# Kernel optimization log

Hardware: AMD Instinct MI355X
Metric: run time of the kernel (lower is better)

The kernel has to match this reference:

```python
import jax, jax.numpy as jnp
import numpy as np

B, IN, NC, O, H = 256, 2048, 1000, 4096, 4  # batch, in_features, num_classes, n_decoders, hidden
NEG_SLOPE = 0.1

def setup_inputs() -> dict:
    key = jax.random.key(0)
    ks = jax.random.split(key, 7)
    s1 = 1.0 / np.sqrt(IN)
    s2 = 1.0 / np.sqrt(H)
    return {
        "x":   jax.random.normal(ks[0], (B, IN), jnp.float32),
        "fcW": jax.random.normal(ks[1], (NC, IN), jnp.float32) * s1,
        "fcb": jax.random.normal(ks[2], (NC,), jnp.float32) * s1,
        "W1":  jax.random.normal(ks[3], (O, IN, H), jnp.float32) * s1,
        "b1":  jax.random.normal(ks[4], (O, H), jnp.float32) * s1,
        "W2":  jax.random.normal(ks[5], (O, H), jnp.float32) * s2,
        "b2":  jax.random.normal(ks[6], (O,), jnp.float32) * s2,
    }

def reference(x, fcW, fcb, W1, b1, W2, b2):
    # fc head: x1 = x @ fcW^T + fcb  -> [B, NC]
    x1 = jnp.einsum("bi,ci->bc", x, fcW) + fcb
    # 4096 tiny MLPs batched into one grouped GEMM:
    # h = leaky_relu(x @ W1_o + b1_o) for each decoder o  -> [B, O, H]
    h = jnp.einsum("bi,oih->boh", x, W1) + b1
    h = jnp.where(h >= 0, h, NEG_SLOPE * h)
    # second layer (H->1) collapses to a weighted reduction -> [B, O]
    x2 = jnp.einsum("boh,oh->bo", h, W2) + b2
    return (x1, x2)
```

## Files before the change

kernel.cpp:

```cpp
#include <hip/hip_runtime.h>


typedef __bf16 bf16_t;
typedef __bf16 bf16x8 __attribute__((ext_vector_type(8)));
typedef __bf16 bf16x4 __attribute__((ext_vector_type(4)));
typedef float  f32x4  __attribute__((ext_vector_type(4)));

#define LDSTR 72

__global__ __launch_bounds__(256, 4)
void fused_dual(const float* __restrict__ x,
                const float* __restrict__ fcW,
                const float* __restrict__ fcb,
                const float* __restrict__ W1,
                const float* __restrict__ b1,
                const float* __restrict__ W2,
                const float* __restrict__ b2,
                float* __restrict__ out)
{
    __shared__ bf16_t lA[64 * LDSTR];
    __shared__ bf16_t lB[64 * LDSTR];

    const int tid = threadIdx.x;
    const int blk = blockIdx.x;
    const int cg  = blk >> 2;
    const int rg  = blk & 3;
    const int m0  = rg * 64;
    const bool is_fc = (cg < 16);
    const int c0  = (is_fc ? cg : cg - 16) * 64;

    const int a_row = tid >> 4;
    const int a_c4  = tid & 15;
    const int b_n  = tid >> 2;
    const int b_kb = tid & 3;

    const float* ap = x + (m0 + a_row) * 2048 + a_c4 * 4;
    const float* bp;
    if (is_fc) {
        int row = c0 + b_n; if (row > 999) row = 999;
        bp = fcW + row * 2048 + b_kb * 16;
    } else {
        const int o = (c0 >> 2) + (b_n >> 2);
        bp = W1 + o * 8192 + b_kb * 64 + (b_n & 3);
    }

    float4 aR[4];
    float  bR[16];

    #pragma unroll
    for (int r = 0; r < 4; ++r) aR[r] = *(const float4*)(ap + r * (16 * 2048));
    if (is_fc) {
        #pragma unroll
        for (int q = 0; q < 4; ++q) {
            float4 t = *(const float4*)(bp + q * 4);
            bR[q*4+0] = t.x; bR[q*4+1] = t.y; bR[q*4+2] = t.z; bR[q*4+3] = t.w;
        }
    } else {
        #pragma unroll
        for (int j = 0; j < 16; ++j) bR[j] = bp[j * 4];
    }

    const int wav  = tid >> 6;
    const int lane = tid & 63;
    const int l15  = lane & 15;
    const int quad = lane >> 4;

    f32x4 acc[4];
    #pragma unroll
    for (int nt = 0; nt < 4; ++nt) acc[nt] = (f32x4){0.f, 0.f, 0.f, 0.f};

    char* lAb = (char*)lA;
    char* lBb = (char*)lB;
    const int aW = (a_row) * (LDSTR * 2) + a_c4 * 8;
    const int bW = b_n * (LDSTR * 2) + b_kb * 32;

    for (int kt = 0; kt < 32; ++kt) {
        __syncthreads();
        #pragma unroll
        for (int r = 0; r < 4; ++r) {
            bf16x4 v;
            v[0] = (bf16_t)aR[r].x; v[1] = (bf16_t)aR[r].y;
            v[2] = (bf16_t)aR[r].z; v[3] = (bf16_t)aR[r].w;
            *(bf16x4*)(lAb + aW + r * (16 * LDSTR * 2)) = v;
        }
        {
            bf16x8 v0, v1;
            #pragma unroll
            for (int j = 0; j < 8; ++j) { v0[j] = (bf16_t)bR[j]; v1[j] = (bf16_t)bR[8 + j]; }
            *(bf16x8*)(lBb + bW)      = v0;
            *(bf16x8*)(lBb + bW + 16) = v1;
        }
        __syncthreads();
        if (kt != 31) {
            ap += 64;
            bp += is_fc ? 64 : 256;
            #pragma unroll
            for (int r = 0; r < 4; ++r) aR[r] = *(const float4*)(ap + r * (16 * 2048));
            if (is_fc) {
                #pragma unroll
                for (int q = 0; q < 4; ++q) {
                    float4 t = *(const float4*)(bp + q * 4);
                    bR[q*4+0] = t.x; bR[q*4+1] = t.y; bR[q*4+2] = t.z; bR[q*4+3] = t.w;
                }
            } else {
                #pragma unroll
                for (int j = 0; j < 16; ++j) bR[j] = bp[j * 4];
            }
        }
        #pragma unroll
        for (int kk = 0; kk < 2; ++kk) {
            bf16x8 af = *(const bf16x8*)(lAb + (wav * 16 + l15) * (LDSTR * 2) + kk * 64 + quad * 16);
            #pragma unroll
            for (int nt = 0; nt < 4; ++nt) {
                bf16x8 bf = *(const bf16x8*)(lBb + (nt * 16 + l15) * (LDSTR * 2) + kk * 64 + quad * 16);
                acc[nt] = __builtin_amdgcn_mfma_f32_16x16x32_bf16(af, bf, acc[nt], 0, 0, 0);
            }
        }
    }

    if (is_fc) {
        #pragma unroll
        for (int nt = 0; nt < 4; ++nt) {
            const int c = c0 + nt * 16 + l15;
            const bool valid = (c < 1000);
            const float bias = fcb[valid ? c : 999];
            #pragma unroll
            for (int r = 0; r < 4; ++r) {
                if (valid) {
                    const int row = m0 + wav * 16 + quad * 4 + r;
                    out[row * 1000 + c] = acc[nt][r] + bias;
                }
            }
        }
    } else {
        float* x2out = out + 256 * 1000;
        #pragma unroll
        for (int nt = 0; nt < 4; ++nt) {
            const int c   = c0 + nt * 16 + l15;
            const float b1v = b1[c];
            const float w2v = W2[c];
            const int o   = c >> 2;
            const float b2v = b2[o];
            #pragma unroll
            for (int r = 0; r < 4; ++r) {
                float h = acc[nt][r] + b1v;
                h = (h >= 0.f) ? h : 0.1f * h;
                float wv = h * w2v;
                wv += __shfl_xor(wv, 1, 64);
                wv += __shfl_xor(wv, 2, 64);
                if ((lane & 3) == 0) {
                    const int row = m0 + wav * 16 + quad * 4 + r;
                    x2out[row * 4096 + o] = wv + b2v;
                }
            }
        }
    }
}

extern "C" void kernel_launch(void* const* d_in, const int* in_sizes, int n_in,
                              void* d_out, int out_size, void* d_ws, size_t ws_size,
                              hipStream_t stream)
{
    (void)in_sizes; (void)n_in; (void)d_ws; (void)ws_size; (void)out_size;
    const float* x   = (const float*)d_in[0];
    const float* fcW = (const float*)d_in[1];
    const float* fcb = (const float*)d_in[2];
    const float* W1  = (const float*)d_in[3];
    const float* b1  = (const float*)d_in[4];
    const float* W2  = (const float*)d_in[5];
    const float* b2  = (const float*)d_in[6];
    fused_dual<<<1088, 256, 0, stream>>>(x, fcW, fcb, W1, b1, W2, b2, (float*)d_out);
}
```

Measured before the change: 293.6 us.

## Double-buffer global prefetch, 2x2 wave tiling, and vectorized W1 loads

Global loads are prefetched two k-tiles ahead using two register sets, so memory latency overlaps with MFMA work. LDS fragments are loaded into registers before the barrier, letting the next tile be staged while MFMAs run. Waves now form a 2x2 arrangement over the 64x64 tile, which reduces the number of B-fragment LDS reads per wave. W1 is read with contiguous float4 loads along IN and transposed while staging into LDS, replacing strided scalar loads. The cost is higher register pressure under launch_bounds(256,4) and more barriers per iteration.

Result: no change. 297.5 us (+1.3%).

```diff
diff --git a/kernel.cpp b/kernel.cpp
--- a/kernel.cpp
+++ b/kernel.cpp
@@ -7,6 +7,7 @@
 typedef float  f32x4  __attribute__((ext_vector_type(4)));
 
 #define LDSTR 72
+#define ROWB  (LDSTR*2)
 
 __global__ __launch_bounds__(256, 4)
 void fused_dual(const float* __restrict__ x,
@@ -20,137 +21,139 @@
 {
     __shared__ bf16_t lA[64 * LDSTR];
     __shared__ bf16_t lB[64 * LDSTR];
+    char* lAb = (char*)lA;
+    char* lBb = (char*)lB;
 
-    const int tid = threadIdx.x;
-    const int blk = blockIdx.x;
-    const int cg  = blk >> 2;
-    const int rg  = blk & 3;
-    const int m0  = rg * 64;
+    const int tid = threadIdx.x, blk = blockIdx.x;
+    const int cg = blk >> 2, rg = blk & 3, m0 = rg * 64;
     const bool is_fc = (cg < 16);
-    const int c0  = (is_fc ? cg : cg - 16) * 64;
+    const int c0 = (is_fc ? cg : cg - 16) * 64;
 
-    const int a_row = tid >> 4;
-    const int a_c4  = tid & 15;
-    const int b_n  = tid >> 2;
-    const int b_kb = tid & 3;
+    const float* aBase = x + (m0 + (tid >> 2)) * 2048 + (tid & 3) * 16;
+    const int aW = (tid >> 2) * ROWB + (tid & 3) * 32;
 
-    const float* ap = x + (m0 + a_row) * 2048 + a_c4 * 4;
-    const float* bp;
+    const float* bBase;
+    int bStride, bW;
     if (is_fc) {
-        int row = c0 + b_n; if (row > 999) row = 999;
-        bp = fcW + row * 2048 + b_kb * 16;
+        int row = c0 + (tid >> 2); if (row > 999) row = 999;
+        bBase = fcW + row * 2048 + (tid & 3) * 16;
+        bStride = 64;
+        bW = (tid >> 2) * ROWB + (tid & 3) * 32;
     } else {
-        const int o = (c0 >> 2) + (b_n >> 2);
-        bp = W1 + o * 8192 + b_kb * 64 + (b_n & 3);
+        bBase = W1 + ((c0 >> 2) + (tid >> 4)) * 8192 + (tid & 15) * 16;
+        bStride = 256;
+        bW = (tid >> 4) * 4 * ROWB + (tid & 15) * 8;
     }
 
-    float4 aR[4];
-    float  bR[16];
+    f32x4 aR0[4], bR0[4], aR1[4], bR1[4];
 
-    #pragma unroll
-    for (int r = 0; r < 4; ++r) aR[r] = *(const float4*)(ap + r * (16 * 2048));
-    if (is_fc) {
-        #pragma unroll
-        for (int q = 0; q < 4; ++q) {
-            float4 t = *(const float4*)(bp + q * 4);
-            bR[q*4+0] = t.x; bR[q*4+1] = t.y; bR[q*4+2] = t.z; bR[q*4+3] = t.w;
+#define ISSUE(AR, BR, TL) do {                                              \
+    const float* _a = aBase + (TL) * 64;                                    \
+    const float* _b = bBase + (TL) * bStride;                               \
+    _Pragma("unroll") for (int q = 0; q < 4; ++q) AR[q] = *(const f32x4*)(_a + q * 4); \
+    _Pragma("unroll") for (int q = 0; q < 4; ++q) BR[q] = *(const f32x4*)(_b + q * 4); \
+} while (0)
+
+#define STAGE(AR, BR) do {                                                  \
+    bf16x8 _va0, _va1;                                                      \
+    _Pragma("unroll") for (int c = 0; c < 4; ++c) {                         \
+        _va0[c] = (bf16_t)AR[0][c]; _va0[4 + c] = (bf16_t)AR[1][c];         \
+        _va1[c] = (bf16_t)AR[2][c]; _va1[4 + c] = (bf16_t)AR[3][c]; }       \
+    *(bf16x8*)(lAb + aW) = _va0; *(bf16x8*)(lAb + aW + 16) = _va1;          \
+    if (is_fc) {                                                            \
+        bf16x8 _vb0, _vb1;                                                  \
+        _Pragma("unroll") for (int c = 0; c < 4; ++c) {                     \
+            _vb0[c] = (bf16_t)BR[0][c]; _vb0[4 + c] = (bf16_t)BR[1][c];     \
+            _vb1[c] = (bf16_t)BR[2][c]; _vb1[4 + c] = (bf16_t)BR[3][c]; }   \
+        *(bf16x8*)(lBb + bW) = _vb0; *(bf16x8*)(lBb + bW + 16) = _vb1;      \
+    } else {                                                                \
+        _Pragma("unroll") for (int h = 0; h < 4; ++h) {                     \
+            bf16x4 _v;                                                      \
+            _Pragma("unroll") for (int q = 0; q < 4; ++q) _v[q] = (bf16_t)BR[q][h]; \
+            *(bf16x4*)(lBb + bW + h * ROWB) = _v; }                         \
+    }                                                                       \
+} while (0)
+
+    const int lane = tid & 63, wav = tid >> 6, l15 = lane & 15, quad = lane >> 4;
+    const int mt0 = (wav & 1) * 2, nt0 = (wav >> 1) * 2;
+
+    f32x4 acc[2][2];
+    acc[0][0] = acc[0][1] = acc[1][0] = acc[1][1] = (f32x4){0.f, 0.f, 0.f, 0.f};
+    bf16x8 af[2][2], bfr[2][2];
+
+#define FRAGS() do {                                                        \
+    _Pragma("unroll") for (int kk = 0; kk < 2; ++kk)                        \
+    _Pragma("unroll") for (int i = 0; i < 2; ++i) {                         \
+        af[kk][i]  = *(const bf16x8*)(lAb + ((mt0 + i) * 16 + l15) * ROWB + kk * 64 + quad * 16); \
+        bfr[kk][i] = *(const bf16x8*)(lBb + ((nt0 + i) * 16 + l15) * ROWB + kk * 64 + quad * 16); \
+    }                                                                       \
+} while (0)
+
+#define MFMA8() do {                                                        \
+    _Pragma("unroll") for (int kk = 0; kk < 2; ++kk)                        \
+    _Pragma("unroll") for (int i = 0; i < 2; ++i)                           \
+    _Pragma("unroll") for (int j = 0; j < 2; ++j)                           \
+        acc[i][j] = __builtin_amdgcn_mfma_f32_16x16x32_bf16(af[kk][i], bfr[kk][j], acc[i][j], 0, 0, 0); \
+} while (0)
+
+    ISSUE(aR0, bR0, 0);
+    ISSUE(aR1, bR1, 1);
+    STAGE(aR0, bR0);
+    ISSUE(aR0, bR0, 2);
+    __syncthreads();
+
+    for (int kt = 0; kt < 32; kt += 2) {
+        FRAGS();
+        __syncthreads();
+        STAGE(aR1, bR1);
+        if (kt + 3 < 32) ISSUE(aR1, bR1, kt + 3);
+        __syncthreads();
+        MFMA8();
+        FRAGS();
+        __syncthreads();
+        if (kt + 1 < 31) {
+            STAGE(aR0, bR0);
+            if (kt + 4 < 32) ISSUE(aR0, bR0, kt + 4);
+            __syncthreads();
         }
-    } else {
-        #pragma unroll
-        for (int j = 0; j < 16; ++j) bR[j] = bp[j * 4];
-    }
-
-    const int wav  = tid >> 6;
-    const int lane = tid & 63;
-    const int l15  = lane & 15;
-    const int quad = lane >> 4;
-
-    f32x4 acc[4];
-    #pragma unroll
-    for (int nt = 0; nt < 4; ++nt) acc[nt] = (f32x4){0.f, 0.f, 0.f, 0.f};
-
-    char* lAb = (char*)lA;
-    char* lBb = (char*)lB;
-    const int aW = (a_row) * (LDSTR * 2) + a_c4 * 8;
-    const int bW = b_n * (LDSTR * 2) + b_kb * 32;
-
-    for (int kt = 0; kt < 32; ++kt) {
-        __syncthreads();
-        #pragma unroll
-        for (int r = 0; r < 4; ++r) {
-            bf16x4 v;
-            v[0] = (bf16_t)aR[r].x; v[1] = (bf16_t)aR[r].y;
-            v[2] = (bf16_t)aR[r].z; v[3] = (bf16_t)aR[r].w;
-            *(bf16x4*)(lAb + aW + r * (16 * LDSTR * 2)) = v;
-        }
-        {
-            bf16x8 v0, v1;
-            #pragma unroll
-            for (int j = 0; j < 8; ++j) { v0[j] = (bf16_t)bR[j]; v1[j] = (bf16_t)bR[8 + j]; }
-            *(bf16x8*)(lBb + bW)      = v0;
-            *(bf16x8*)(lBb + bW + 16) = v1;
-        }
-        __syncthreads();
-        if (kt != 31) {
-            ap += 64;
-            bp += is_fc ? 64 : 256;
-            #pragma unroll
-            for (int r = 0; r < 4; ++r) aR[r] = *(const float4*)(ap + r * (16 * 2048));
-            if (is_fc) {
-                #pragma unroll
-                for (int q = 0; q < 4; ++q) {
-                    float4 t = *(const float4*)(bp + q * 4);
-                    bR[q*4+0] = t.x; bR[q*4+1] = t.y; bR[q*4+2] = t.z; bR[q*4+3] = t.w;
-                }
-            } else {
-                #pragma unroll
-                for (int j = 0; j < 16; ++j) bR[j] = bp[j * 4];
-            }
-        }
-        #pragma unroll
-        for (int kk = 0; kk < 2; ++kk) {
-            bf16x8 af = *(const bf16x8*)(lAb + (wav * 16 + l15) * (LDSTR * 2) + kk * 64 + quad * 16);
-            #pragma unroll
-            for (int nt = 0; nt < 4; ++nt) {
-                bf16x8 bf = *(const bf16x8*)(lBb + (nt * 16 + l15) * (LDSTR * 2) + kk * 64 + quad * 16);
-                acc[nt] = __builtin_amdgcn_mfma_f32_16x16x32_bf16(af, bf, acc[nt], 0, 0, 0);
-            }
-        }
+        MFMA8();
     }
 
     if (is_fc) {
         #pragma unroll
-        for (int nt = 0; nt < 4; ++nt) {
-            const int c = c0 + nt * 16 + l15;
+        for (int j = 0; j < 2; ++j) {
+            const int c = c0 + (nt0 + j) * 16 + l15;
             const bool valid = (c < 1000);
             const float bias = fcb[valid ? c : 999];
             #pragma unroll
-            for (int r = 0; r < 4; ++r) {
+            for (int i = 0; i < 2; ++i)
+            #pragma unroll
+            for (int r = 0; r < 4; ++r)
                 if (valid) {
-                    const int row = m0 + wav * 16 + quad * 4 + r;
-                    out[row * 1000 + c] = acc[nt][r] + bias;
+                    const int row = m0 + (mt0 + i) * 16 + quad * 4 + r;
+                    out[row * 1000 + c] = acc[i][j][r] + bias;
                 }
-            }
         }
     } else {
-        float* x2out = out + 256 * 1000;
+        float* x2 = out + 256 * 1000;
         #pragma unroll
-        for (int nt = 0; nt < 4; ++nt) {
-            const int c   = c0 + nt * 16 + l15;
-            const float b1v = b1[c];
-            const float w2v = W2[c];
-            const int o   = c >> 2;
+        for (int j = 0; j < 2; ++j) {
+            const int c = c0 + (nt0 + j) * 16 + l15;
+            const float b1v = b1[c], w2v = W2[c];
+            const int o = c >> 2;
             const float b2v = b2[o];
             #pragma unroll
+            for (int i = 0; i < 2; ++i)
+            #pragma unroll
             for (int r = 0; r < 4; ++r) {
-                float h = acc[nt][r] + b1v;
+                float h = acc[i][j][r] + b1v;
                 h = (h >= 0.f) ? h : 0.1f * h;
                 float wv = h * w2v;
                 wv += __shfl_xor(wv, 1, 64);
                 wv += __shfl_xor(wv, 2, 64);
                 if ((lane & 3) == 0) {
-                    const int row = m0 + wav * 16 + quad * 4 + r;
-                    x2out[row * 4096 + o] = wv + b2v;
+                    const int row = m0 + (mt0 + i) * 16 + quad * 4 + r;
+                    x2[row * 4096 + o] = wv + b2v;
                 }
             }
         }
```

## Stage fp32 tiles via direct global-to-LDS DMA and convert to bf16 on read

Applied to the files above, without the earlier changes.

Tiles of x and of the weights (fcW or W1) now go straight from global memory into LDS as fp32 slabs using global_load_lds, replacing the register staging and bf16 conversion before the LDS store. Conversion to bf16 happens when fragments are read from LDS, and each wave now computes a 2x2 grid of MFMA tiles instead of a 1x4 strip. Block indices are swizzled across groups of 8, and the decoder output is staged in LDS so it can be written with coalesced 16-byte stores. LDS use and LDS read traffic double because data is held as fp32. The loop still has no double buffering, so each load is exposed between the two barriers.

New measurement: 302.2 us. +2.9%, slower.

```diff
diff --git a/kernel.cpp b/kernel.cpp
--- a/kernel.cpp
+++ b/kernel.cpp
@@ -1,12 +1,18 @@
 #include <hip/hip_runtime.h>
+#include <stdint.h>
 
 
 typedef __bf16 bf16_t;
 typedef __bf16 bf16x8 __attribute__((ext_vector_type(8)));
-typedef __bf16 bf16x4 __attribute__((ext_vector_type(4)));
 typedef float  f32x4  __attribute__((ext_vector_type(4)));
 
-#define LDSTR 72
+#define AS1 __attribute__((address_space(1)))
+#define AS3 __attribute__((address_space(3)))
+#define SLAB 1040
+
+__device__ __forceinline__ void dma16(const float* g, AS3 char* lds_base) {
+    __builtin_amdgcn_global_load_lds((const AS1 void*)g, (AS3 void*)lds_base, 16, 0, 0);
+}
 
 __global__ __launch_bounds__(256, 4)
 void fused_dual(const float* __restrict__ x,
@@ -18,142 +24,149 @@
                 const float* __restrict__ b2,
                 float* __restrict__ out)
 {
-    __shared__ bf16_t lA[64 * LDSTR];
-    __shared__ bf16_t lB[64 * LDSTR];
+    __shared__ __align__(16) char lA[16 * SLAB];
+    __shared__ __align__(16) char lB[16 * SLAB];
+    AS3 char* lA3 = (AS3 char*)lA;
+    AS3 char* lB3 = (AS3 char*)lB;
 
-    const int tid = threadIdx.x;
-    const int blk = blockIdx.x;
-    const int cg  = blk >> 2;
-    const int rg  = blk & 3;
-    const int m0  = rg * 64;
+    const int tid  = threadIdx.x;
+    const int lane = tid & 63, w = tid >> 6;
+    const int l15  = lane & 15, quad = lane >> 4;
+
+    const int idx = blockIdx.x;
+    const int wid = (idx & 7) * 136 + (idx >> 3);
+    const int cg = wid >> 2, rg = wid & 3, m0 = rg * 64;
     const bool is_fc = (cg < 16);
-    const int c0  = (is_fc ? cg : cg - 16) * 64;
+    const int c0 = (is_fc ? cg : cg - 16) * 64;
 
-    const int a_row = tid >> 4;
-    const int a_c4  = tid & 15;
-    const int b_n  = tid >> 2;
-    const int b_kb = tid & 3;
-
-    const float* ap = x + (m0 + a_row) * 2048 + a_c4 * 4;
-    const float* bp;
-    if (is_fc) {
-        int row = c0 + b_n; if (row > 999) row = 999;
-        bp = fcW + row * 2048 + b_kb * 16;
-    } else {
-        const int o = (c0 >> 2) + (b_n >> 2);
-        bp = W1 + o * 8192 + b_kb * 64 + (b_n & 3);
+    const float* aG = x + (m0 + w * 16 + (lane >> 4)) * 2048 + (lane & 15) * 4;
+    const float* bG = W1 + ((c0 >> 2) + w * 4) * 8192 + lane * 4;
+    const float* bF0; const float* bF1; const float* bF2; const float* bF3;
+    {
+        int r0 = c0 + w * 16 + (lane >> 4);
+        int ra = r0;      if (ra > 999) ra = 999;
+        int rb = r0 + 4;  if (rb > 999) rb = 999;
+        int rc = r0 + 8;  if (rc > 999) rc = 999;
+        int rd = r0 + 12; if (rd > 999) rd = 999;
+        bF0 = fcW + ra * 2048 + (lane & 15) * 4;
+        bF1 = fcW + rb * 2048 + (lane & 15) * 4;
+        bF2 = fcW + rc * 2048 + (lane & 15) * 4;
+        bF3 = fcW + rd * 2048 + (lane & 15) * 4;
     }
 
-    float4 aR[4];
-    float  bR[16];
+    const int mt0 = (w >> 1) * 2, nt0 = (w & 1) * 2;
 
-    #pragma unroll
-    for (int r = 0; r < 4; ++r) aR[r] = *(const float4*)(ap + r * (16 * 2048));
-    if (is_fc) {
-        #pragma unroll
-        for (int q = 0; q < 4; ++q) {
-            float4 t = *(const float4*)(bp + q * 4);
-            bR[q*4+0] = t.x; bR[q*4+1] = t.y; bR[q*4+2] = t.z; bR[q*4+3] = t.w;
-        }
-    } else {
-        #pragma unroll
-        for (int j = 0; j < 16; ++j) bR[j] = bp[j * 4];
-    }
-
-    const int wav  = tid >> 6;
-    const int lane = tid & 63;
-    const int l15  = lane & 15;
-    const int quad = lane >> 4;
-
-    f32x4 acc[4];
-    #pragma unroll
-    for (int nt = 0; nt < 4; ++nt) acc[nt] = (f32x4){0.f, 0.f, 0.f, 0.f};
-
-    char* lAb = (char*)lA;
-    char* lBb = (char*)lB;
-    const int aW = (a_row) * (LDSTR * 2) + a_c4 * 8;
-    const int bW = b_n * (LDSTR * 2) + b_kb * 32;
+    f32x4 acc[2][2];
+    acc[0][0] = acc[0][1] = acc[1][0] = acc[1][1] = (f32x4){0.f, 0.f, 0.f, 0.f};
 
     for (int kt = 0; kt < 32; ++kt) {
         __syncthreads();
+        const int ka = kt * 64;
         #pragma unroll
-        for (int r = 0; r < 4; ++r) {
-            bf16x4 v;
-            v[0] = (bf16_t)aR[r].x; v[1] = (bf16_t)aR[r].y;
-            v[2] = (bf16_t)aR[r].z; v[3] = (bf16_t)aR[r].w;
-            *(bf16x4*)(lAb + aW + r * (16 * LDSTR * 2)) = v;
-        }
-        {
-            bf16x8 v0, v1;
+        for (int q = 0; q < 4; ++q)
+            dma16(aG + q * 8192 + ka, lA3 + (w * 4 + q) * SLAB);
+        if (is_fc) {
+            dma16(bF0 + ka, lB3 + (w * 4 + 0) * SLAB);
+            dma16(bF1 + ka, lB3 + (w * 4 + 1) * SLAB);
+            dma16(bF2 + ka, lB3 + (w * 4 + 2) * SLAB);
+            dma16(bF3 + ka, lB3 + (w * 4 + 3) * SLAB);
+        } else {
             #pragma unroll
-            for (int j = 0; j < 8; ++j) { v0[j] = (bf16_t)bR[j]; v1[j] = (bf16_t)bR[8 + j]; }
-            *(bf16x8*)(lBb + bW)      = v0;
-            *(bf16x8*)(lBb + bW + 16) = v1;
+            for (int q = 0; q < 4; ++q)
+                dma16(bG + q * 8192 + kt * 256, lB3 + (w * 4 + q) * SLAB);
         }
         __syncthreads();
-        if (kt != 31) {
-            ap += 64;
-            bp += is_fc ? 64 : 256;
+
+        bf16x8 af[2][2], bf[2][2];
+        #pragma unroll
+        for (int i = 0; i < 2; ++i)
+        #pragma unroll
+        for (int kk = 0; kk < 2; ++kk) {
+            const int arow = (mt0 + i) * 16 + l15;
+            const char* p = lA + (arow >> 2) * SLAB + (arow & 3) * 256 + kk * 128 + quad * 32;
+            f32x4 u0 = *(const f32x4*)p;
+            f32x4 u1 = *(const f32x4*)(p + 16);
             #pragma unroll
-            for (int r = 0; r < 4; ++r) aR[r] = *(const float4*)(ap + r * (16 * 2048));
-            if (is_fc) {
+            for (int c = 0; c < 4; ++c) { af[i][kk][c] = (bf16_t)u0[c]; af[i][kk][4 + c] = (bf16_t)u1[c]; }
+        }
+        if (is_fc) {
+            #pragma unroll
+            for (int j = 0; j < 2; ++j)
+            #pragma unroll
+            for (int kk = 0; kk < 2; ++kk) {
+                const int brow = (nt0 + j) * 16 + l15;
+                const char* p = lB + (brow >> 2) * SLAB + (brow & 3) * 256 + kk * 128 + quad * 32;
+                f32x4 u0 = *(const f32x4*)p;
+                f32x4 u1 = *(const f32x4*)(p + 16);
                 #pragma unroll
-                for (int q = 0; q < 4; ++q) {
-                    float4 t = *(const float4*)(bp + q * 4);
-                    bR[q*4+0] = t.x; bR[q*4+1] = t.y; bR[q*4+2] = t.z; bR[q*4+3] = t.w;
-                }
-            } else {
+                for (int c = 0; c < 4; ++c) { bf[j][kk][c] = (bf16_t)u0[c]; bf[j][kk][4 + c] = (bf16_t)u1[c]; }
+            }
+        } else {
+            #pragma unroll
+            for (int j = 0; j < 2; ++j)
+            #pragma unroll
+            for (int kk = 0; kk < 2; ++kk) {
+                const int n = (nt0 + j) * 16 + l15;
+                const char* p = lB + (n >> 2) * SLAB + (n & 3) * 4 + kk * 512 + quad * 128;
                 #pragma unroll
-                for (int j = 0; j < 16; ++j) bR[j] = bp[j * 4];
+                for (int jj = 0; jj < 8; ++jj)
+                    bf[j][kk][jj] = (bf16_t)*(const float*)(p + jj * 16);
             }
         }
         #pragma unroll
-        for (int kk = 0; kk < 2; ++kk) {
-            bf16x8 af = *(const bf16x8*)(lAb + (wav * 16 + l15) * (LDSTR * 2) + kk * 64 + quad * 16);
-            #pragma unroll
-            for (int nt = 0; nt < 4; ++nt) {
-                bf16x8 bf = *(const bf16x8*)(lBb + (nt * 16 + l15) * (LDSTR * 2) + kk * 64 + quad * 16);
-                acc[nt] = __builtin_amdgcn_mfma_f32_16x16x32_bf16(af, bf, acc[nt], 0, 0, 0);
-            }
-        }
+        for (int kk = 0; kk < 2; ++kk)
+        #pragma unroll
+        for (int i = 0; i < 2; ++i)
+        #pragma unroll
+        for (int j = 0; j < 2; ++j)
+            acc[i][j] = __builtin_amdgcn_mfma_f32_16x16x32_bf16(af[i][kk], bf[j][kk], acc[i][j], 0, 0, 0);
     }
 
     if (is_fc) {
         #pragma unroll
-        for (int nt = 0; nt < 4; ++nt) {
-            const int c = c0 + nt * 16 + l15;
+        for (int j = 0; j < 2; ++j) {
+            const int c = c0 + (nt0 + j) * 16 + l15;
             const bool valid = (c < 1000);
             const float bias = fcb[valid ? c : 999];
             #pragma unroll
-            for (int r = 0; r < 4; ++r) {
+            for (int i = 0; i < 2; ++i)
+            #pragma unroll
+            for (int r = 0; r < 4; ++r)
                 if (valid) {
-                    const int row = m0 + wav * 16 + quad * 4 + r;
-                    out[row * 1000 + c] = acc[nt][r] + bias;
+                    const int row = m0 + (mt0 + i) * 16 + quad * 4 + r;
+                    out[row * 1000 + c] = acc[i][j][r] + bias;
                 }
-            }
         }
     } else {
-        float* x2out = out + 256 * 1000;
+        float* x2 = out + 256 * 1000;
+        const int o0 = (cg - 16) * 16;
+        __syncthreads();
+        float* xs = (float*)lA;
         #pragma unroll
-        for (int nt = 0; nt < 4; ++nt) {
-            const int c   = c0 + nt * 16 + l15;
-            const float b1v = b1[c];
-            const float w2v = W2[c];
-            const int o   = c >> 2;
+        for (int j = 0; j < 2; ++j) {
+            const int c = c0 + (nt0 + j) * 16 + l15;
+            const float b1v = b1[c], w2v = W2[c];
+            const int o = c >> 2;
             const float b2v = b2[o];
             #pragma unroll
+            for (int i = 0; i < 2; ++i)
+            #pragma unroll
             for (int r = 0; r < 4; ++r) {
-                float h = acc[nt][r] + b1v;
+                float h = acc[i][j][r] + b1v;
                 h = (h >= 0.f) ? h : 0.1f * h;
                 float wv = h * w2v;
                 wv += __shfl_xor(wv, 1, 64);
                 wv += __shfl_xor(wv, 2, 64);
                 if ((lane & 3) == 0) {
-                    const int row = m0 + wav * 16 + quad * 4 + r;
-                    x2out[row * 4096 + o] = wv + b2v;
+                    const int row = (mt0 + i) * 16 + quad * 4 + r;
+                    xs[row * 16 + (o - o0)] = wv + b2v;
                 }
             }
         }
+        __syncthreads();
+        const int row = tid >> 2, part = tid & 3;
+        f32x4 v = *(const f32x4*)(lA + row * 64 + part * 16);
+        *(f32x4*)(x2 + (m0 + row) * 4096 + o0 + part * 4) = v;
     }
 }
 
```
